# Performance work log

Measured on AMD Instinct MI355X. Metric: run time of the kernel, lower is better.

Reference implementation:

```python
import jax, jax.numpy as jnp
import numpy as np

N_TOKENS = 8192
D_MODEL = 1024
D_HIDDEN = 2 * D_MODEL
N_EXPERTS = 16
TOP_K = 2


def setup_inputs() -> dict:
    key = jax.random.key(0)
    ks = jax.random.split(key, 6)
    s_in = 1.0 / np.sqrt(D_MODEL)
    s_hid = 1.0 / np.sqrt(D_HIDDEN)
    return {
        "x": jax.random.normal(ks[0], (N_TOKENS, D_MODEL), dtype=jnp.float32),
        # gate: Linear(d_model, n_experts, bias=False); stored as [E, d] like torch weight
        "Wg": jax.random.uniform(ks[1], (N_EXPERTS, D_MODEL), jnp.float32, -s_in, s_in),
        # per-expert MLP params, stacked on leading expert axis; W laid out [in, out]
        "W1": jax.random.uniform(ks[2], (N_EXPERTS, D_MODEL, D_HIDDEN), jnp.float32, -s_in, s_in),
        "b1": jax.random.uniform(ks[3], (N_EXPERTS, D_HIDDEN), jnp.float32, -s_in, s_in),
        "W2": jax.random.uniform(ks[4], (N_EXPERTS, D_HIDDEN, D_MODEL), jnp.float32, -s_hid, s_hid),
        "b2": jax.random.uniform(ks[5], (N_EXPERTS, D_MODEL), jnp.float32, -s_hid, s_hid),
    }


def reference(x, Wg, W1, b1, W2, b2):
    # Router: top-k logits, softmax over the k selected logits (in fp32)
    logits = x @ Wg.T                                  # [N, E]
    topk_vals, topk_idx = jax.lax.top_k(logits, TOP_K)  # [N, K]
    rw = jax.nn.softmax(topk_vals.astype(jnp.float32), axis=-1).astype(x.dtype)
    # Combine top-k weights into per-(token, expert) weights [N, E]
    cw = (jax.nn.one_hot(topk_idx, N_EXPERTS, dtype=x.dtype) * rw[..., None]).sum(axis=1)
    # Dense per-expert MLP, weighted combine (equivalent to gather/scatter index_add_)
    out = jnp.zeros_like(x)
    for e in range(N_EXPERTS):
        h = jax.nn.relu(x @ W1[e] + b1[e])             # [N, D_HIDDEN]
        out = out + (h @ W2[e] + b2[e]) * cw[:, e:e + 1]
    return out
```

## Files before the change

kernel.cpp:

```cpp
#include <hip/hip_runtime.h>
#include <hip/hip_bf16.h>
#include <stdint.h>

#define NTOK 8192
#define DM   1024
#define DH   2048
#define NE   16

#define NWRK  768
#define QCAP1 2048
#define QCAP2 1024

typedef float  f32x4  __attribute__((ext_vector_type(4)));
typedef __bf16 bf16x8 __attribute__((ext_vector_type(8)));

__device__ __forceinline__ unsigned short f2bf(float f) {
  union { __bf16 b; unsigned short u; } c; c.b = (__bf16)f; return c.u;
}

__device__ __forceinline__ void glds16(const void* g, void* l) {
  __builtin_amdgcn_global_load_lds(
      (const __attribute__((address_space(1))) void*)g,
      (__attribute__((address_space(3))) void*)l, 16, 0, 0);
}

__global__ __launch_bounds__(256) void router_kernel(
    const float* __restrict__ x, const float* __restrict__ Wg,
    unsigned short* __restrict__ xb, int* __restrict__ eidx,
    float* __restrict__ ewt)
{
  const int lane = threadIdx.x & 63;
  const int wave = threadIdx.x >> 6;
  const int t = blockIdx.x * 4 + wave;
  const float* xr = x + (size_t)t * DM;

  float4 xv[4];
#pragma unroll
  for (int c = 0; c < 4; ++c)
    xv[c] = *(const float4*)(xr + c * 256 + lane * 4);

  unsigned short* xbr = xb + (size_t)t * DM;
#pragma unroll
  for (int c = 0; c < 4; ++c) {
    ushort4 u;
    u.x = f2bf(xv[c].x); u.y = f2bf(xv[c].y);
    u.z = f2bf(xv[c].z); u.w = f2bf(xv[c].w);
    *(ushort4*)(xbr + c * 256 + lane * 4) = u;
  }

  float acc[NE];
#pragma unroll
  for (int e = 0; e < NE; ++e) acc[e] = 0.f;
#pragma unroll
  for (int e = 0; e < NE; ++e) {
#pragma unroll
    for (int c = 0; c < 4; ++c) {
      float4 wv = *(const float4*)(Wg + e * DM + c * 256 + lane * 4);
      acc[e] += xv[c].x * wv.x + xv[c].y * wv.y + xv[c].z * wv.z + xv[c].w * wv.w;
    }
  }
#pragma unroll
  for (int e = 0; e < NE; ++e) {
    float v = acc[e];
    v += __shfl_xor(v, 1);  v += __shfl_xor(v, 2);  v += __shfl_xor(v, 4);
    v += __shfl_xor(v, 8);  v += __shfl_xor(v, 16); v += __shfl_xor(v, 32);
    acc[e] = v;
  }
  if (lane == 0) {
    float v0 = -1e30f; int i0 = 0;
#pragma unroll
    for (int e = 0; e < NE; ++e) if (acc[e] > v0) { v0 = acc[e]; i0 = e; }
    float v1 = -1e30f; int i1 = 0;
#pragma unroll
    for (int e = 0; e < NE; ++e) if (e != i0 && acc[e] > v1) { v1 = acc[e]; i1 = e; }
    float p = expf(v1 - v0);
    float s = 1.f / (1.f + p);
    eidx[2 * t] = i0; eidx[2 * t + 1] = i1;
    ewt[2 * t] = s;   ewt[2 * t + 1] = p * s;
  }
}

__global__ __launch_bounds__(1024) void planprep_kernel(
    const int* __restrict__ eidx, const float* __restrict__ ewt,
    int* __restrict__ cnt, int* __restrict__ offv,
    int* __restrict__ tok, float* __restrict__ wtl,
    int* __restrict__ wl1, int* __restrict__ wl2,
    int* __restrict__ qn1, int* __restrict__ qn2,
    int* __restrict__ qc1, int* __restrict__ qc2,
    const float* __restrict__ W1, unsigned short* __restrict__ w1t,
    const float* __restrict__ W2, unsigned short* __restrict__ w2t)
{
  __shared__ float t[4][64][68];
  __shared__ int wcnt[16][NE];
  __shared__ int wbase[16][NE];
  __shared__ int offs[NE];
  __shared__ int s_nmt[NE];
  __shared__ int s_pnmt[NE + 1];

  if (blockIdx.x != 0) {
    const int idx = blockIdx.x - 1;
    const int tg  = threadIdx.x >> 8;
    const int t8  = threadIdx.x & 255;
    const float* W; unsigned short* WT; int K, N, tt, bx, by;
    if (idx < 2048) {
      W = W1; WT = w1t; K = DM; N = DH;
      tt = idx * 4 + tg;
      int r = tt & 511; bx = r & 31; by = r >> 5;
    } else {
      W = W2; WT = w2t; K = DH; N = DM;
      tt = (idx - 2048) * 4 + tg;
      int r = tt & 511; bx = r & 15; by = r >> 4;
    }
    const int bz = tt >> 9;
    const int k0 = by * 64, n0 = bx * 64;
    const int tr = t8 >> 2;
    const int tc = (t8 & 3) * 16;
    const float* src = W + ((size_t)bz * K + k0) * N + n0;
#pragma unroll
    for (int j = 0; j < 4; ++j) {
      float4 v = *(const float4*)(src + (size_t)tr * N + tc + j * 4);
      t[tg][tc + j * 4 + 0][tr] = v.x;
      t[tg][tc + j * 4 + 1][tr] = v.y;
      t[tg][tc + j * 4 + 2][tr] = v.z;
      t[tg][tc + j * 4 + 3][tr] = v.w;
    }
    __syncthreads();
    unsigned short* dst = WT + ((size_t)bz * N + n0) * K + k0;
#pragma unroll
    for (int j = 0; j < 4; ++j) {
      float4 v = *(const float4*)(&t[tg][tr][tc + j * 4]);
      ushort4 u;
      u.x = f2bf(v.x); u.y = f2bf(v.y); u.z = f2bf(v.z); u.w = f2bf(v.w);
      *(ushort4*)(dst + (size_t)tr * K + tc + j * 4) = u;
    }
    return;
  }

  const int tid  = threadIdx.x;
  const int wave = tid >> 6;
  const int lane = tid & 63;
  const unsigned long long below = (1ull << lane) - 1ull;

  int   pe[16];
  float pw[16];
  int   count[NE];
#pragma unroll
  for (int e = 0; e < NE; ++e) count[e] = 0;
#pragma unroll
  for (int r = 0; r < 16; ++r) {
    int p = wave * 1024 + r * 64 + lane;
    pe[r] = eidx[p];
    pw[r] = ewt[p];
#pragma unroll
    for (int e = 0; e < NE; ++e) {
      unsigned long long m = __ballot(pe[r] == e);
      count[e] += (int)__popcll(m);
    }
  }
  if (lane == 0) {
#pragma unroll
    for (int e = 0; e < NE; ++e) wcnt[wave][e] = count[e];
  }
  __syncthreads();

  if (tid == 0) {
    int s = 0;
    s_pnmt[0] = 0;
    for (int e = 0; e < NE; ++e) {
      offs[e] = s;
      int tcnt = 0;
      for (int w = 0; w < 16; ++w) { wbase[w][e] = tcnt; tcnt += wcnt[w][e]; }
      cnt[e] = tcnt; offv[e] = s; s += tcnt;
      int nmt = (tcnt + 127) >> 7;
      s_nmt[e] = nmt;
      s_pnmt[e + 1] = s_pnmt[e] + nmt;
    }
    offv[NE] = s;
  }
  __syncthreads();

  if (tid < 8) {
    qn1[tid] = (s_nmt[tid] + s_nmt[tid + 8]) * 16;
    qn2[tid] = (s_nmt[tid] + s_nmt[tid + 8]) * 8;
    qc1[tid] = 0;
    qc2[tid] = 0;
  }

  {
    const int totmt = s_pnmt[NE];
    const int T1 = totmt * 16;
    for (int i = tid; i < T1; i += 1024) {
      int gmt = i >> 4, p = i & 15;
      int e = 0;
      while (s_pnmt[e + 1] <= gmt) ++e;
      int mt  = gmt - s_pnmt[e];
      int nmt = s_nmt[e];
      int xx   = e & 7;
      int base = (e < 8) ? 0 : s_nmt[e - 8] * 16;
      wl1[xx * QCAP1 + base + p * nmt + mt] = (e << 16) | (mt << 8) | p;
    }
    const int T2 = totmt * 8;
    for (int i = tid; i < T2; i += 1024) {
      int gmt = i >> 3, p = i & 7;
      int e = 0;
      while (s_pnmt[e + 1] <= gmt) ++e;
      int mt  = gmt - s_pnmt[e];
      int nmt = s_nmt[e];
      int h0  = (nmt + 1) >> 1;
      int pos_e = (mt < h0) ? (p * h0 + mt)
                            : (h0 * 8 + p * (nmt - h0) + (mt - h0));
      int xx   = e & 7;
      int base = (e < 8) ? 0 : s_nmt[e - 8] * 8;
      wl2[xx * QCAP2 + base + pos_e] = (e << 16) | (mt << 8) | p;
    }
  }

  int run[NE];
#pragma unroll
  for (int e = 0; e < NE; ++e) run[e] = 0;
#pragma unroll
  for (int r = 0; r < 16; ++r) {
    int p = wave * 1024 + r * 64 + lane;
#pragma unroll
    for (int e = 0; e < NE; ++e) {
      unsigned long long m = __ballot(pe[r] == e);
      if (pe[r] == e) {
        int rank = (int)__popcll(m & below);
        int slot = offs[e] + wbase[wave][e] + run[e] + rank;
        tok[slot] = p >> 1;
        wtl[slot] = pw[r];
      }
      run[e] += (int)__popcll(m);
    }
  }
}

template<int GATHER, int EPI, int KDIM, int NDIM, int QCAP>
__global__ __launch_bounds__(256, 3) void gemm_kernel(
    const unsigned short* __restrict__ Abase,
    const unsigned short* __restrict__ BT,
    const float* __restrict__ bias,
    const int* __restrict__ cnt, const int* __restrict__ offv,
    const int* __restrict__ tok, const float* __restrict__ wtl,
    const int* __restrict__ wl, const int* __restrict__ qn,
    int* __restrict__ qc, void* __restrict__ outp)
{
  __shared__ unsigned short Al[128 * 64];
  __shared__ unsigned short Bl[128 * 64];
  __shared__ int s_j;

  const int xcd = blockIdx.x & 7;
  const int* q_ = wl + xcd * QCAP;
  const int myqn = qn[xcd];

  const int tid  = threadIdx.x;
  const int lane = tid & 63;
  const int wave = tid >> 6;
  const int wr = wave >> 1;
  const int wc = wave & 1;

  const int lr = lane >> 3;
  const int lc = lane & 7;
  const int sc = (lc ^ lr) * 8;
  const int qq   = lane >> 4;
  const int ln15 = lane & 15;
  const int swz  = ln15 & 7;

  for (;;) {
    if (tid == 0) s_j = atomicAdd(&qc[xcd], 1);
    __syncthreads();
    const int j = s_j;
    if (j >= myqn) return;
    const int v = q_[j];

    const int e  = (v >> 16) & 0xff;
    const int m0 = ((v >> 8) & 0xff) * 128;
    const int n0 = (v & 0xff) * 128;
    const int count = cnt[e];
    const int o     = offv[e];

    const unsigned short* aptr[4];
    const unsigned short* bptr[4];
#pragma unroll
    for (int ii = 0; ii < 4; ++ii) {
      int i = wave * 4 + ii;
      int r = i * 8 + lr;
      int m = m0 + r; if (m > count - 1) m = count - 1;
      size_t arow = GATHER ? (size_t)tok[o + m] : (size_t)(o + m);
      aptr[ii] = Abase + arow * KDIM + sc;
      bptr[ii] = BT + ((size_t)e * NDIM + n0 + r) * KDIM + sc;
    }

    f32x4 acc[4][4];
#pragma unroll
    for (int a = 0; a < 4; ++a)
#pragma unroll
      for (int b = 0; b < 4; ++b) acc[a][b] = 0.f;

    for (int k0 = 0; k0 < KDIM; k0 += 64) {
#pragma unroll
      for (int ii = 0; ii < 4; ++ii) {
        int i = wave * 4 + ii;
        glds16(aptr[ii] + k0, &Al[i * 512]);
        glds16(bptr[ii] + k0, &Bl[i * 512]);
      }
      __syncthreads();
#pragma unroll
      for (int kk = 0; kk < 2; ++kk) {
        bf16x8 af[4], bg[4];
        const int ch = (kk * 4 + qq) ^ swz;
#pragma unroll
        for (int a = 0; a < 4; ++a) {
          int r = wr * 64 + a * 16 + ln15;
          af[a] = *(const bf16x8*)(&Al[r * 64 + ch * 8]);
        }
#pragma unroll
        for (int b = 0; b < 4; ++b) {
          int r = wc * 64 + b * 16 + ln15;
          bg[b] = *(const bf16x8*)(&Bl[r * 64 + ch * 8]);
        }
#pragma unroll
        for (int a = 0; a < 4; ++a)
#pragma unroll
          for (int b = 0; b < 4; ++b)
            acc[a][b] = __builtin_amdgcn_mfma_f32_16x16x32_bf16(af[a], bg[b], acc[a][b], 0, 0, 0);
      }
      __syncthreads();
    }

    float bn[4];
#pragma unroll
    for (int b = 0; b < 4; ++b)
      bn[b] = bias[(size_t)e * NDIM + n0 + wc * 64 + b * 16 + ln15];

    if (EPI == 0) {
      unsigned short* hout = (unsigned short*)outp;
#pragma unroll
      for (int a = 0; a < 4; ++a)
#pragma unroll
        for (int rg = 0; rg < 4; ++rg) {
          int r = wr * 64 + a * 16 + qq * 4 + rg;
          int m = m0 + r;
          if (m < count) {
            size_t slot = (size_t)(o + m);
#pragma unroll
            for (int b = 0; b < 4; ++b) {
              float v2 = acc[a][b][rg] + bn[b];
              v2 = v2 > 0.f ? v2 : 0.f;
              hout[slot * NDIM + n0 + wc * 64 + b * 16 + ln15] = f2bf(v2);
            }
          }
        }
    } else {
      float* obase = (float*)outp;
#pragma unroll
      for (int a = 0; a < 4; ++a)
#pragma unroll
        for (int rg = 0; rg < 4; ++rg) {
          int r = wr * 64 + a * 16 + qq * 4 + rg;
          int m = m0 + r;
          if (m < count) {
            int slot = o + m;
            int tk = tok[slot];
            float w = wtl[slot];
#pragma unroll
            for (int b = 0; b < 4; ++b) {
              float v2 = (acc[a][b][rg] + bn[b]) * w;
              atomicAdd(&obase[(size_t)tk * NDIM + n0 + wc * 64 + b * 16 + ln15], v2);
            }
          }
        }
    }
  }
}

extern "C" void kernel_launch(void* const* d_in, const int* in_sizes, int n_in,
                              void* d_out, int out_size, void* d_ws, size_t ws_size,
                              hipStream_t stream) {
  const float* x  = (const float*)d_in[0];
  const float* Wg = (const float*)d_in[1];
  const float* W1 = (const float*)d_in[2];
  const float* b1 = (const float*)d_in[3];
  const float* W2 = (const float*)d_in[4];
  const float* b2 = (const float*)d_in[5];

  constexpr size_t OFF_CNT  = 0;
  constexpr size_t OFF_OFF  = 256;
  constexpr size_t OFF_QN1  = 512;
  constexpr size_t OFF_QN2  = 544;
  constexpr size_t OFF_QC1  = 576;
  constexpr size_t OFF_QC2  = 608;
  constexpr size_t OFF_WL1  = 4096;
  constexpr size_t OFF_WL2  = OFF_WL1 + (size_t)8 * QCAP1 * 4;
  constexpr size_t OFF_EIDX = OFF_WL2 + (size_t)8 * QCAP2 * 4;
  constexpr size_t OFF_EWT  = OFF_EIDX + (size_t)NTOK * 2 * 4;
  constexpr size_t OFF_TOK  = OFF_EWT  + (size_t)NTOK * 2 * 4;
  constexpr size_t OFF_WTL  = OFF_TOK  + (size_t)NTOK * 2 * 4;
  constexpr size_t OFF_XB   = (size_t)1 << 20;
  constexpr size_t OFF_W1T  = OFF_XB  + (size_t)NTOK * DM * 2;
  constexpr size_t OFF_W2T  = OFF_W1T + (size_t)NE * DM * DH * 2;
  constexpr size_t OFF_H    = OFF_W2T + (size_t)NE * DH * DM * 2;
  constexpr size_t REQ      = OFF_H   + (size_t)NTOK * 2 * DH * 2;
  static_assert(OFF_WTL + (size_t)NTOK * 2 * 4 <= OFF_XB, "ws layout overlap");

  if (ws_size < REQ) {
    hipMemsetAsync(d_out, 0, (size_t)out_size * 4, stream);
    return;
  }

  char* ws = (char*)d_ws;
  int*   cnt    = (int*)(ws + OFF_CNT);
  int*   offv   = (int*)(ws + OFF_OFF);
  int*   qn1    = (int*)(ws + OFF_QN1);
  int*   qn2    = (int*)(ws + OFF_QN2);
  int*   qc1    = (int*)(ws + OFF_QC1);
  int*   qc2    = (int*)(ws + OFF_QC2);
  int*   wl1    = (int*)(ws + OFF_WL1);
  int*   wl2    = (int*)(ws + OFF_WL2);
  int*   eidx   = (int*)(ws + OFF_EIDX);
  float* ewt    = (float*)(ws + OFF_EWT);
  int*   tok    = (int*)(ws + OFF_TOK);
  float* wtl    = (float*)(ws + OFF_WTL);
  unsigned short* xb   = (unsigned short*)(ws + OFF_XB);
  unsigned short* w1t  = (unsigned short*)(ws + OFF_W1T);
  unsigned short* w2t  = (unsigned short*)(ws + OFF_W2T);
  unsigned short* hbuf = (unsigned short*)(ws + OFF_H);

  hipMemsetAsync(d_out, 0, (size_t)out_size * 4, stream);

  router_kernel<<<NTOK / 4, 256, 0, stream>>>(x, Wg, xb, eidx, ewt);
  planprep_kernel<<<4097, 1024, 0, stream>>>(
      eidx, ewt, cnt, offv, tok, wtl, wl1, wl2, qn1, qn2, qc1, qc2,
      W1, w1t, W2, w2t);

  gemm_kernel<1, 0, DM, DH, QCAP1><<<NWRK, 256, 0, stream>>>(
      xb, w1t, b1, cnt, offv, tok, wtl, wl1, qn1, qc1, hbuf);
  gemm_kernel<0, 1, DH, DM, QCAP2><<<NWRK, 256, 0, stream>>>(
      hbuf, w2t, b2, cnt, offv, tok, wtl, wl2, qn2, qc2, (float*)d_out);
}
```

Measured before the change: 357.6 us.

## Overlap W2 transpose-convert with first expert GEMM via interleaved work items

The W2 fp32-to-bf16 transpose is moved out of the planprep kernel and into the first grouped GEMM as extra work-queue items. These items are interleaved with GEMM tiles so the memory-bound conversion overlaps with the compute-bound GEMM1. The first GEMM also gets more workers and a higher occupancy bound (4 waves per SIMD instead of 3) and a larger queue capacity. This adds branching inside the persistent loop and risks GEMM1 tiles competing with transpose traffic for bandwidth.

```diff
diff --git a/kernel.cpp b/kernel.cpp
--- a/kernel.cpp
+++ b/kernel.cpp
@@ -7,9 +7,10 @@
 #define DH   2048
 #define NE   16
 
-#define NWRK  768
-#define QCAP1 2048
-#define QCAP2 1024
+#define NWRK1 1024
+#define NWRK2 768
+#define QCAP1 4096
+#define QCAP2 2048
 
 typedef float  f32x4  __attribute__((ext_vector_type(4)));
 typedef __bf16 bf16x8 __attribute__((ext_vector_type(8)));
@@ -87,8 +88,7 @@
     int* __restrict__ wl1, int* __restrict__ wl2,
     int* __restrict__ qn1, int* __restrict__ qn2,
     int* __restrict__ qc1, int* __restrict__ qc2,
-    const float* __restrict__ W1, unsigned short* __restrict__ w1t,
-    const float* __restrict__ W2, unsigned short* __restrict__ w2t)
+    const float* __restrict__ W1, unsigned short* __restrict__ w1t)
 {
   __shared__ float t[4][64][68];
   __shared__ int wcnt[16][NE];
@@ -101,37 +101,29 @@
     const int idx = blockIdx.x - 1;
     const int tg  = threadIdx.x >> 8;
     const int t8  = threadIdx.x & 255;
-    const float* W; unsigned short* WT; int K, N, tt, bx, by;
-    if (idx < 2048) {
-      W = W1; WT = w1t; K = DM; N = DH;
-      tt = idx * 4 + tg;
-      int r = tt & 511; bx = r & 31; by = r >> 5;
-    } else {
-      W = W2; WT = w2t; K = DH; N = DM;
-      tt = (idx - 2048) * 4 + tg;
-      int r = tt & 511; bx = r & 15; by = r >> 4;
-    }
-    const int bz = tt >> 9;
+    const int tt = idx * 4 + tg;
+    const int r = tt & 511;
+    const int bx = r & 31, by = r >> 5, bz = tt >> 9;
     const int k0 = by * 64, n0 = bx * 64;
     const int tr = t8 >> 2;
     const int tc = (t8 & 3) * 16;
-    const float* src = W + ((size_t)bz * K + k0) * N + n0;
+    const float* src = W1 + ((size_t)bz * DM + k0) * DH + n0;
 #pragma unroll
     for (int j = 0; j < 4; ++j) {
-      float4 v = *(const float4*)(src + (size_t)tr * N + tc + j * 4);
+      float4 v = *(const float4*)(src + (size_t)tr * DH + tc + j * 4);
       t[tg][tc + j * 4 + 0][tr] = v.x;
       t[tg][tc + j * 4 + 1][tr] = v.y;
       t[tg][tc + j * 4 + 2][tr] = v.z;
       t[tg][tc + j * 4 + 3][tr] = v.w;
     }
     __syncthreads();
-    unsigned short* dst = WT + ((size_t)bz * N + n0) * K + k0;
+    unsigned short* dst = w1t + ((size_t)bz * DH + n0) * DM + k0;
 #pragma unroll
     for (int j = 0; j < 4; ++j) {
       float4 v = *(const float4*)(&t[tg][tr][tc + j * 4]);
       ushort4 u;
       u.x = f2bf(v.x); u.y = f2bf(v.y); u.z = f2bf(v.z); u.w = f2bf(v.w);
-      *(ushort4*)(dst + (size_t)tr * K + tc + j * 4) = u;
+      *(ushort4*)(dst + (size_t)tr * DM + tc + j * 4) = u;
     }
     return;
   }
@@ -180,7 +172,7 @@
   __syncthreads();
 
   if (tid < 8) {
-    qn1[tid] = (s_nmt[tid] + s_nmt[tid + 8]) * 16;
+    qn1[tid] = (s_nmt[tid] + s_nmt[tid + 8]) * 16 + 256;
     qn2[tid] = (s_nmt[tid] + s_nmt[tid + 8]) * 8;
     qc1[tid] = 0;
     qc2[tid] = 0;
@@ -196,8 +188,19 @@
       int mt  = gmt - s_pnmt[e];
       int nmt = s_nmt[e];
       int xx   = e & 7;
+      int G    = (s_nmt[xx] + s_nmt[xx + 8]) * 16;
+      int mn   = G < 256 ? G : 256;
       int base = (e < 8) ? 0 : s_nmt[e - 8] * 16;
-      wl1[xx * QCAP1 + base + p * nmt + mt] = (e << 16) | (mt << 8) | p;
+      int r    = base + p * nmt + mt;
+      int slot = (r < mn) ? 2 * r : r + mn;
+      wl1[xx * QCAP1 + slot] = (e << 16) | (mt << 8) | p;
+    }
+    for (int i = tid; i < 8 * 256; i += 1024) {
+      int xx = i >> 8, k = i & 255;
+      int G  = (s_nmt[xx] + s_nmt[xx + 8]) * 16;
+      int mn = G < 256 ? G : 256;
+      int slot = (k < mn) ? 2 * k + 1 : k + G;
+      wl1[xx * QCAP1 + slot] = 0x40000000 | (xx * 256 + k);
     }
     const int T2 = totmt * 8;
     for (int i = tid; i < T2; i += 1024) {
@@ -235,18 +238,20 @@
   }
 }
 
-template<int GATHER, int EPI, int KDIM, int NDIM, int QCAP>
-__global__ __launch_bounds__(256, 3) void gemm_kernel(
+template<int GATHER, int EPI, int TPW2, int MINW, int KDIM, int NDIM, int QCAP>
+__global__ __launch_bounds__(256, MINW) void gemm_kernel(
     const unsigned short* __restrict__ Abase,
     const unsigned short* __restrict__ BT,
     const float* __restrict__ bias,
     const int* __restrict__ cnt, const int* __restrict__ offv,
     const int* __restrict__ tok, const float* __restrict__ wtl,
     const int* __restrict__ wl, const int* __restrict__ qn,
-    int* __restrict__ qc, void* __restrict__ outp)
+    int* __restrict__ qc, void* __restrict__ outp,
+    const float* __restrict__ W2src, unsigned short* __restrict__ w2dst)
 {
-  __shared__ unsigned short Al[128 * 64];
-  __shared__ unsigned short Bl[128 * 64];
+  __shared__ __align__(16) char smem[32768];
+  unsigned short* Al = (unsigned short*)smem;
+  unsigned short* Bl = (unsigned short*)(smem + 16384);
   __shared__ int s_j;
 
   const int xcd = blockIdx.x & 7;
@@ -272,6 +277,39 @@
     const int j = s_j;
     if (j >= myqn) return;
     const int v = q_[j];
+
+    if (TPW2 && (v & 0x40000000)) {
+      float (*tp)[68] = (float(*)[68])smem;
+      const int tg4 = v & 0xffff;
+      const int tr = tid >> 2;
+      const int tc = (tid & 3) * 16;
+      for (int s = 0; s < 4; ++s) {
+        int tt = tg4 * 4 + s;
+        int r = tt & 511;
+        int bx = r & 15, by = r >> 4, bz = tt >> 9;
+        int k0 = by * 64, n0 = bx * 64;
+        const float* src = W2src + ((size_t)bz * DH + k0) * DM + n0;
+#pragma unroll
+        for (int jj = 0; jj < 4; ++jj) {
+          float4 vv = *(const float4*)(src + (size_t)tr * DM + tc + jj * 4);
+          tp[tc + jj * 4 + 0][tr] = vv.x;
+          tp[tc + jj * 4 + 1][tr] = vv.y;
+          tp[tc + jj * 4 + 2][tr] = vv.z;
+          tp[tc + jj * 4 + 3][tr] = vv.w;
+        }
+        __syncthreads();
+        unsigned short* dst = w2dst + ((size_t)bz * DM + n0) * DH + k0;
+#pragma unroll
+        for (int jj = 0; jj < 4; ++jj) {
+          float4 vv = *(const float4*)(&tp[tr][tc + jj * 4]);
+          ushort4 u;
+          u.x = f2bf(vv.x); u.y = f2bf(vv.y); u.z = f2bf(vv.z); u.w = f2bf(vv.w);
+          *(ushort4*)(dst + (size_t)tr * DH + tc + jj * 4) = u;
+        }
+        __syncthreads();
+      }
+      continue;
+    }
 
     const int e  = (v >> 16) & 0xff;
     const int m0 = ((v >> 8) & 0xff) * 128;
@@ -429,12 +467,13 @@
   hipMemsetAsync(d_out, 0, (size_t)out_size * 4, stream);
 
   router_kernel<<<NTOK / 4, 256, 0, stream>>>(x, Wg, xb, eidx, ewt);
-  planprep_kernel<<<4097, 1024, 0, stream>>>(
+  planprep_kernel<<<2049, 1024, 0, stream>>>(
       eidx, ewt, cnt, offv, tok, wtl, wl1, wl2, qn1, qn2, qc1, qc2,
-      W1, w1t, W2, w2t);
-
-  gemm_kernel<1, 0, DM, DH, QCAP1><<<NWRK, 256, 0, stream>>>(
-      xb, w1t, b1, cnt, offv, tok, wtl, wl1, qn1, qc1, hbuf);
-  gemm_kernel<0, 1, DH, DM, QCAP2><<<NWRK, 256, 0, stream>>>(
-      hbuf, w2t, b2, cnt, offv, tok, wtl, wl2, qn2, qc2, (float*)d_out);
-}
+      W1, w1t);
+
+  gemm_kernel<1, 0, 1, 4, DM, DH, QCAP1><<<NWRK1, 256, 0, stream>>>(
+      xb, w1t, b1, cnt, offv, tok, wtl, wl1, qn1, qc1, hbuf, W2, w2t);
+  gemm_kernel<0, 1, 0, 3, DH, DM, QCAP2><<<NWRK2, 256, 0, stream>>>(
+      hbuf, w2t, b2, cnt, offv, tok, wtl, wl2, qn2, qc2, (float*)d_out,
+      nullptr, nullptr);
+}
```

After: 369.3 us. +3.3%, slower.
